# Kernel optimization log

Hardware: AMD Instinct MI355X
Metric: run time of the kernel (lower is better)

## Reference

```python
import jax, jax.numpy as jnp
import numpy as np
import math

N = 50000      # nodes
E = 800000     # edges
IN = 64        # in_channels
HID = 128      # hidden_channels
OUT = 64       # out_channels
RATIO = 0.8
K = int(math.ceil(RATIO * N))  # 40000 nodes kept after TopKPooling


def setup_inputs() -> dict:
    key = jax.random.key(0)
    ks = jax.random.split(key, 12)
    x = jax.random.normal(ks[0], (N, IN), jnp.float32)
    edge_index = jax.random.randint(ks[1], (2, E), 0, N, dtype=jnp.int32)
    batch = jnp.zeros((N,), jnp.int32)  # single graph

    def glorot(k, fi, fo):
        return jax.random.normal(k, (fi, fo), jnp.float32) * (1.0 / np.sqrt(fi))

    W1 = glorot(ks[2], IN, HID);  b1 = jnp.zeros((HID,), jnp.float32)
    pool_w = jax.random.normal(ks[3], (HID,), jnp.float32) * (1.0 / np.sqrt(HID))
    W2 = glorot(ks[4], HID, OUT); b2 = jnp.zeros((OUT,), jnp.float32)
    W3 = glorot(ks[5], OUT, HID); b3 = jnp.zeros((HID,), jnp.float32)
    W4 = glorot(ks[6], HID, IN);  b4 = jnp.zeros((IN,), jnp.float32)
    return dict(x=x, edge_index=edge_index, batch=batch,
                W1=W1, b1=b1, pool_w=pool_w, W2=W2, b2=b2,
                W3=W3, b3=b3, W4=W4, b4=b4)


def gcn_conv(x, src, dst, ew, W, b, n):
    """PyG GCNConv: D^{-1/2}(A+I)D^{-1/2} X W + b; ew is a 0/1 edge mask."""
    h = x @ W                                             # [n, d_out]
    deg = 1.0 + jax.ops.segment_sum(ew, dst, num_segments=n)  # self-loop adds 1
    dis = jax.lax.rsqrt(deg)
    norm = dis[src] * dis[dst] * ew                       # [E]
    agg = jax.ops.segment_sum(norm[:, None] * h[src], dst, num_segments=n)
    agg = agg + h * (dis * dis)[:, None]                  # self-loop: norm = 1/deg
    return agg + b


def reference(x, edge_index, batch, W1, b1, pool_w, W2, b2, W3, b3, W4, b4):
    src, dst = edge_index[0], edge_index[1]
    ew = jnp.ones((E,), x.dtype)

    # conv1 + relu
    h = jax.nn.relu(gcn_conv(x, src, dst, ew, W1, b1, N))

    # TopKPooling(ratio=0.8): score = tanh(x.w/||w||), keep top-K, scale x by score
    score = jnp.tanh(h @ pool_w / jnp.linalg.norm(pool_w))  # [N]
    vals, perm = jax.lax.top_k(score, K)
    hp = h[perm] * vals[:, None]                            # [K, HID]
    # remap edges to pooled node ids; drop edges touching removed nodes via mask
    new_idx = jnp.full((N,), -1, jnp.int32).at[perm].set(jnp.arange(K, dtype=jnp.int32))
    ns, nd = new_idx[src], new_idx[dst]
    valid = ((ns >= 0) & (nd >= 0)).astype(x.dtype)
    ns = jnp.maximum(ns, 0)
    nd = jnp.maximum(nd, 0)

    h2 = jax.nn.relu(gcn_conv(hp, ns, nd, valid, W2, b2, K))
    h3 = jax.nn.relu(gcn_conv(h2, ns, nd, valid, W3, b3, K))
    h4 = gcn_conv(h3, ns, nd, valid, W4, b4, K)             # [K, IN]

    # global_mean_pool over the (single) graph -> [1, IN]
    return jnp.mean(h4, axis=0, keepdims=True)
```

## Files before the change

kernel.cpp:

```cpp
#include <hip/hip_runtime.h>
#include <hip/hip_bf16.h>
#include <stdint.h>

#define N_NODES 50000
#define N_EDGES 800000
#define K_KEEP  40000
#define BKT     196
#define BCAP    6144

typedef unsigned long long u64;
typedef unsigned int u32;
typedef unsigned short u16;
typedef __hip_bfloat16 bf16;
typedef __hip_bfloat162 bf16x2;
typedef __attribute__((ext_vector_type(8))) short short8;
typedef __attribute__((ext_vector_type(8))) unsigned short ushort8;
typedef __attribute__((ext_vector_type(4))) float f32x4;

struct Ctl {
  u64 prefix;
  u32 kremain;
  u32 cnt;
  float inv_norm;
  u32 isfp32;
  u32 done;
  u32 pad;
  u32 gen;
  u32 done2;
  u32 hist[256];
};

__device__ __forceinline__ float bf2f(bf16 v) { return __bfloat162float(v); }
__device__ __forceinline__ float bfbits2f(unsigned short u) {
  return __uint_as_float(((u32)u) << 16);
}
__device__ __forceinline__ float loadF(const void* p, size_t i, bool f32) {
  return f32 ? ((const float*)p)[i] : bf2f(((const bf16*)p)[i]);
}
__device__ __forceinline__ short f2bf_bits(float f) {
  bf16 t = __float2bfloat16(f);
  return *(const short*)&t;
}

__device__ __forceinline__ void gather_row8_pre(const ushort8* __restrict__ H, int d, int lane,
                                                const int* __restrict__ rowstart,
                                                const int* __restrict__ len,
                                                const int* __restrict__ csr,
                                                float* acc)
{
  ushort8 v = H[(size_t)d * 8 + lane];
  #pragma unroll
  for (int c = 0; c < 8; ++c) acc[c] = bfbits2f(v[c]);
  int i = rowstart[d];
  int i1 = len ? (i + len[d]) : rowstart[d + 1];
  for (; i + 8 <= i1; i += 8) {
    int s0 = csr[i],     s1 = csr[i + 1], s2 = csr[i + 2], s3 = csr[i + 3];
    int s4 = csr[i + 4], s5 = csr[i + 5], s6 = csr[i + 6], s7 = csr[i + 7];
    ushort8 v0 = H[(size_t)s0 * 8 + lane];
    ushort8 v1 = H[(size_t)s1 * 8 + lane];
    ushort8 v2 = H[(size_t)s2 * 8 + lane];
    ushort8 v3 = H[(size_t)s3 * 8 + lane];
    ushort8 v4 = H[(size_t)s4 * 8 + lane];
    ushort8 v5 = H[(size_t)s5 * 8 + lane];
    ushort8 v6 = H[(size_t)s6 * 8 + lane];
    ushort8 v7 = H[(size_t)s7 * 8 + lane];
    #pragma unroll
    for (int c = 0; c < 8; ++c) {
      acc[c] += (bfbits2f(v0[c]) + bfbits2f(v1[c]))
              + (bfbits2f(v2[c]) + bfbits2f(v3[c]));
      acc[c] += (bfbits2f(v4[c]) + bfbits2f(v5[c]))
              + (bfbits2f(v6[c]) + bfbits2f(v7[c]));
    }
  }
  for (; i + 4 <= i1; i += 4) {
    int s0 = csr[i], s1 = csr[i + 1], s2 = csr[i + 2], s3 = csr[i + 3];
    ushort8 v0 = H[(size_t)s0 * 8 + lane];
    ushort8 v1 = H[(size_t)s1 * 8 + lane];
    ushort8 v2 = H[(size_t)s2 * 8 + lane];
    ushort8 v3 = H[(size_t)s3 * 8 + lane];
    #pragma unroll
    for (int c = 0; c < 8; ++c) {
      acc[c] += (bfbits2f(v0[c]) + bfbits2f(v1[c]))
              + (bfbits2f(v2[c]) + bfbits2f(v3[c]));
    }
  }
  for (; i < i1; ++i) {
    int s = csr[i];
    ushort8 vv = H[(size_t)s * 8 + lane];
    #pragma unroll
    for (int c = 0; c < 8; ++c) acc[c] += bfbits2f(vv[c]);
  }
}

__device__ __forceinline__ void gather_wave_partial(const ushort8* __restrict__ H, int d,
                                                    int slot, int unit,
                                                    const int* __restrict__ rowstart,
                                                    const int* __restrict__ len,
                                                    const int* __restrict__ csr,
                                                    float* acc,
                                                    float* __restrict__ cvec, float dd)
{
  #pragma unroll
  for (int c = 0; c < 8; ++c) acc[c] = 0.f;
  if (slot == 0) {
    ushort8 v = H[(size_t)d * 8 + unit];
    #pragma unroll
    for (int c = 0; c < 8; ++c) acc[c] = bfbits2f(v[c]);
  }
  int i0 = rowstart[d];
  int i1 = i0 + len[d];
  int i = i0 + slot;
  for (; i + 8 < i1; i += 16) {
    int sa = csr[i], sb = csr[i + 8];
    if (cvec && unit == 0) {
      atomicAdd(&cvec[sa], dd);
      atomicAdd(&cvec[sb], dd);
    }
    ushort8 va = H[(size_t)sa * 8 + unit];
    ushort8 vb = H[(size_t)sb * 8 + unit];
    #pragma unroll
    for (int c = 0; c < 8; ++c) acc[c] += bfbits2f(va[c]) + bfbits2f(vb[c]);
  }
  if (i < i1) {
    int s = csr[i];
    if (cvec && unit == 0) atomicAdd(&cvec[s], dd);
    ushort8 vv = H[(size_t)s * 8 + unit];
    #pragma unroll
    for (int c = 0; c < 8; ++c) acc[c] += bfbits2f(vv[c]);
  }
}


__global__ void init_kernel(const unsigned short* __restrict__ x16,
                            int* __restrict__ bucket_cur, int* __restrict__ detcnt,
                            Ctl* ctl, float* __restrict__ cvec) {
  __shared__ u32 dsh[256];
  int i = blockIdx.x * 256 + threadIdx.x;
  if (i < BKT) bucket_cur[i] = i * BCAP;
  if (i < K_KEEP) cvec[i] = 0.f;
  if (blockIdx.x == 0) {
    ctl->hist[threadIdx.x] = 0u;
    if (threadIdx.x == 0) {
      ctl->prefix = 0ull; ctl->kremain = K_KEEP; ctl->cnt = 0u;
      ctl->done = 0u; ctl->pad = 0u; ctl->gen = 0u; ctl->done2 = 0u;
    }
  }
  if (blockIdx.x < 64) {
    int base = blockIdx.x * 2048;
    u32 c = 0;
    for (int j = threadIdx.x; j < 2048; j += 256) {
      u32 h = x16[base + j];
      if ((h & 0x7F80u) == 0x7F80u) c++;
    }
    dsh[threadIdx.x] = c;
    __syncthreads();
    for (int s = 128; s > 0; s >>= 1) {
      if (threadIdx.x < s) dsh[threadIdx.x] += dsh[threadIdx.x + s];
      __syncthreads();
    }
    if (threadIdx.x == 0) detcnt[blockIdx.x] = (int)dsh[0];
  }
}


__global__ void bucket_scatter_kernel(const int* __restrict__ src, const int* __restrict__ dst,
                                      int* __restrict__ bucket_cur, u32* __restrict__ bucketbuf,
                                      const int* __restrict__ detcnt, const void* __restrict__ pw,
                                      Ctl* ctl)
{
  __shared__ u32 hist[BKT];
  __shared__ u32 base[BKT];
  __shared__ int f32sh;
  __shared__ float ns[128];
  const int tid = threadIdx.x;
  const int e0 = blockIdx.x * 2048;

  if (tid < 64) {
    int dc = detcnt[tid];
    for (int off = 32; off; off >>= 1) dc += __shfl_down(dc, off);
    if (tid == 0) f32sh = (dc >= 16) ? 1 : 0;
  }
  for (int t = tid; t < BKT; t += 256) hist[t] = 0;
  __syncthreads();
  const bool f32in = f32sh != 0;

  int dreg[8], sreg[8];
  const int eb = e0 + tid * 8;
  if (e0 + 2048 <= N_EDGES) {
    const int4* d4 = (const int4*)(dst + eb);
    const int4* s4 = (const int4*)(src + eb);
    int4 da = d4[0], db = d4[1];
    int4 sa = s4[0], sb = s4[1];
    dreg[0] = da.x; dreg[1] = da.y; dreg[2] = da.z; dreg[3] = da.w;
    dreg[4] = db.x; dreg[5] = db.y; dreg[6] = db.z; dreg[7] = db.w;
    sreg[0] = sa.x; sreg[1] = sa.y; sreg[2] = sa.z; sreg[3] = sa.w;
    sreg[4] = sb.x; sreg[5] = sb.y; sreg[6] = sb.z; sreg[7] = sb.w;
  } else {
    #pragma unroll
    for (int j = 0; j < 8; ++j) {
      int e = eb + j;
      if (e < N_EDGES) { dreg[j] = dst[e]; sreg[j] = src[e]; }
      else             { dreg[j] = -1;     sreg[j] = 0;      }
    }
  }
  #pragma unroll
  for (int j = 0; j < 8; ++j)
    if (dreg[j] >= 0) atomicAdd(&hist[dreg[j] >> 8], 1u);
  __syncthreads();
  for (int t = tid; t < BKT; t += 256) {
    u32 c = hist[t];
    base[t] = c ? (u32)atomicAdd(&bucket_cur[t], (int)c) : 0u;
    hist[t] = 0;
  }
  __syncthreads();
  #pragma unroll
  for (int j = 0; j < 8; ++j) {
    if (dreg[j] >= 0) {
      int d = dreg[j];
      int b = d >> 8;
      u32 pos = base[b] + atomicAdd(&hist[b], 1u);
      bucketbuf[pos] = ((u32)sreg[j] << 8) | (u32)(d & 255);
    }
  }
  if (blockIdx.x == 0) {
    if (tid < 128) { float v = loadF(pw, tid, f32in); ns[tid] = v * v; }
    __syncthreads();
    for (int s = 64; s > 0; s >>= 1) {
      if (tid < s) ns[tid] += ns[tid + s];
      __syncthreads();
    }
    if (tid == 0) {
      ctl->inv_norm = 1.0f / sqrtf(ns[0]);
      ctl->isfp32 = f32in ? 1u : 0u;
    }
  }
}


__global__ void csr_from_buckets_kernel(const u32* __restrict__ bucketbuf, const int* __restrict__ bucket_cur,
                                        int* __restrict__ rowstart, float* __restrict__ dis,
                                        int* __restrict__ csr,
                                        const void* __restrict__ x, ushort8* __restrict__ xbf,
                                        const Ctl* __restrict__ ctl)
{
  __shared__ u32 cnt[256];
  __shared__ u32 loc[256];
  __shared__ u32 cur[256];
  __shared__ float disS[256];
  const int b = blockIdx.x;
  const int tid = threadIdx.x;

  int v = (tid < BKT) ? (bucket_cur[tid] - tid * BCAP) : 0;
  loc[tid] = (u32)v;
  __syncthreads();
  for (int off = 1; off < 256; off <<= 1) {
    u32 t = (tid >= off) ? loc[tid - off] : 0;
    __syncthreads();
    loc[tid] += t;
    __syncthreads();
  }
  const int bc = bucket_cur[b] - b * BCAP;
  const int off0 = (int)loc[b] - bc;
  if (b == BKT - 1 && tid == 0) rowstart[N_NODES] = (int)loc[BKT - 1];
  __syncthreads();

  const u32* buf = bucketbuf + (size_t)b * BCAP;
  cnt[tid] = 0;
  __syncthreads();
  for (int i = tid; i < bc; i += 256) atomicAdd(&cnt[buf[i] & 255u], 1u);
  __syncthreads();
  u32 c = cnt[tid];
  loc[tid] = c;
  __syncthreads();
  for (int off = 1; off < 256; off <<= 1) {
    u32 t = (tid >= off) ? loc[tid - off] : 0;
    __syncthreads();
    loc[tid] += t;
    __syncthreads();
  }
  int node = b * 256 + tid;
  u32 excl = loc[tid] - c;
  float ddv = rsqrtf(1.0f + (float)c);
  disS[tid] = ddv;
  if (node < N_NODES) {
    rowstart[node] = off0 + (int)excl;
    dis[node] = ddv;
  }
  cur[tid] = off0 + excl;
  __syncthreads();
  for (int i = tid; i < bc; i += 256) {
    u32 p = buf[i];
    u32 pos = atomicAdd(&cur[p & 255u], 1u);
    csr[pos] = (int)(p >> 8);
  }
  {
    const bool f32in = ctl->isfp32 != 0;
    if (f32in) {
      const float* xf = (const float*)x;
      for (int u = tid; u < 2048; u += 256) {
        int r = u >> 3, lane = u & 7;
        int d = b * 256 + r;
        if (d < N_NODES) {
          float sc = disS[r];
          ushort8 o;
          #pragma unroll
          for (int c2 = 0; c2 < 8; ++c2)
            o[c2] = (u16)f2bf_bits(xf[(size_t)d * 64 + lane * 8 + c2] * sc);
          xbf[(size_t)d * 8 + lane] = o;
        }
      }
    } else {
      const ushort8* xi = (const ushort8*)x;
      for (int u = tid; u < 2048; u += 256) {
        int r = u >> 3, lane = u & 7;
        int d = b * 256 + r;
        if (d < N_NODES) {
          float sc = disS[r];
          ushort8 vv = xi[(size_t)d * 8 + lane];
          ushort8 o;
          #pragma unroll
          for (int c2 = 0; c2 < 8; ++c2)
            o[c2] = (u16)f2bf_bits(bfbits2f(vv[c2]) * sc);
          xbf[(size_t)d * 8 + lane] = o;
        }
      }
    }
  }
}


__global__ void gather_h2_kernel(const bf16* __restrict__ P, const int* __restrict__ rowstart,
                                 const int* __restrict__ len, const int* __restrict__ csr,
                                 const float* __restrict__ dis,
                                 const void* __restrict__ b, const Ctl* __restrict__ ctl,
                                 bf16* __restrict__ P2, float* __restrict__ cvec, int M)
{
  const bool f32 = ctl->isfp32 != 0;
  const int tid = threadIdx.x;
  const int d = blockIdx.x * 4 + (tid >> 6);
  const int lane = tid & 63;
  const int slot = lane >> 3, unit = lane & 7;
  const ushort8* H = (const ushort8*)P;
  const float dd = dis[d];
  float acc[8];
  gather_wave_partial(H, d, slot, unit, rowstart, len, csr, acc, cvec, dd);
  #pragma unroll
  for (int m = 8; m < 64; m <<= 1)
    #pragma unroll
    for (int c = 0; c < 8; ++c) acc[c] += __shfl_xor(acc[c], m);
  if (slot == 0) {
    ushort8 outv;
    #pragma unroll
    for (int c = 0; c < 8; ++c) {
      float h = acc[c] * dd + loadF(b, 8 * unit + c, f32);
      outv[c] = (u16)f2bf_bits(fmaxf(h, 0.f) * dd);
    }
    ((ushort8*)P2)[(size_t)d * 8 + unit] = outv;
  }
}


__global__ void gemm_in_kernel(const ushort8* __restrict__ xbf,
                               const int* __restrict__ rowstart, const int* __restrict__ csr,
                               const float* __restrict__ dis,
                               const void* __restrict__ W, const void* __restrict__ b,
                               const void* __restrict__ pw,
                               bf16* __restrict__ Y, const Ctl* __restrict__ ctl,
                               float* __restrict__ score, u64* __restrict__ keys)
{
  __shared__ short Xs[64 * 72];
  __shared__ short Wt[128 * 72];
  __shared__ float bs[128];
  __shared__ float ps[128];
  const bool f32 = ctl->isfp32 != 0;
  const int tid = threadIdx.x;
  const int row0 = blockIdx.x * 64;

  if (!f32) {
    const short8* W8 = (const short8*)W;
    for (int i = tid; i < 1024; i += 256) {
      int k = i >> 4, nb = i & 15;
      short8 v = W8[i];
      #pragma unroll
      for (int j = 0; j < 8; ++j) Wt[(nb * 8 + j) * 72 + k] = v[j];
    }
  } else {
    for (int i = tid; i < 64 * 128; i += 256) {
      int k = i >> 7, n = i & 127;
      Wt[n * 72 + k] = f2bf_bits(((const float*)W)[i]);
    }
  }
  for (int u = tid; u < 512; u += 256) {
    int r = u >> 3, lane = u & 7;
    int d = row0 + r;
    float acc[8];
    short8 outv;
    if (d < N_NODES) {
      gather_row8_pre(xbf, d, lane, rowstart, nullptr, csr, acc);
      float dd = dis[d];
      #pragma unroll
      for (int c = 0; c < 8; ++c) outv[c] = f2bf_bits(acc[c] * dd);
    } else {
      #pragma unroll
      for (int c = 0; c < 8; ++c) outv[c] = 0;
    }
    *(short8*)&Xs[r * 72 + lane * 8] = outv;
  }
  for (int i = tid; i < 128; i += 256) { bs[i] = loadF(b, i, f32); ps[i] = loadF(pw, i, f32); }
  __syncthreads();

  const int lane = tid & 63;
  const int w = tid >> 6;
  const int l16 = lane & 15;
  const int quad = lane >> 4;
  f32x4 acc[8];
  #pragma unroll
  for (int ct = 0; ct < 8; ++ct) acc[ct] = (f32x4){0.f, 0.f, 0.f, 0.f};
  const int arow = w * 16 + l16;
  #pragma unroll
  for (int kc = 0; kc < 2; ++kc) {
    short8 a = *(short8*)&Xs[arow * 72 + kc * 32 + quad * 8];
    #pragma unroll
    for (int ct = 0; ct < 8; ++ct) {
      short8 bb = *(short8*)&Wt[(ct * 16 + l16) * 72 + kc * 32 + quad * 8];
      acc[ct] = __builtin_amdgcn_mfma_f32_16x16x32_bf16(a, bb, acc[ct], 0, 0, 0);
    }
  }
  float inv_norm = ctl->inv_norm;
  #pragma unroll
  for (int r = 0; r < 4; ++r) {
    int gr = row0 + w * 16 + quad * 4 + r;
    float p = 0.f;
    #pragma unroll
    for (int ct = 0; ct < 8; ++ct) {
      int col = ct * 16 + l16;
      float h = acc[ct][r] + bs[col];
      if (gr < N_NODES) Y[(size_t)gr * 128 + col] = __float2bfloat16(h);
      p += fmaxf(h, 0.f) * ps[col];
    }
    p += __shfl_down(p, 8, 16);
    p += __shfl_down(p, 4, 16);
    p += __shfl_down(p, 2, 16);
    p += __shfl_down(p, 1, 16);
    if (l16 == 0 && gr < N_NODES) {
      float sc = tanhf(p * inv_norm);
      score[gr] = sc;
      u32 u = __float_as_uint(sc);
      u = (u & 0x80000000u) ? ~u : (u | 0x80000000u);
      keys[gr] = (((u64)u) << 16) | (u64)(0xFFFFu - (u32)gr);
    }
  }
}

__global__ void gemm_128_64_kernel(const bf16* __restrict__ X, const void* __restrict__ W,
                                   bf16* __restrict__ Y, const Ctl* __restrict__ ctl,
                                   int M, int relu_x,
                                   const int* __restrict__ kept, const float* __restrict__ score,
                                   const float* __restrict__ prescale)
{
  __shared__ short Xs[64 * 136];
  __shared__ short Wt[64 * 136];
  __shared__ int keptS[64];
  __shared__ float scS[64];
  const bool f32 = ctl->isfp32 != 0;
  const int tid = threadIdx.x;
  const int row0 = blockIdx.x * 64;

  if (kept) {
    for (int i = tid; i < 64; i += 256) {
      int o = kept[row0 + i];
      keptS[i] = o;
      scS[i] = score[o];
    }
  }
  __syncthreads();

  if (!f32) {
    const short8* W8 = (const short8*)W;
    for (int i = tid; i < 1024; i += 256) {
      int k = i >> 3, nb = i & 7;
      short8 v = W8[i];
      #pragma unroll
      for (int j = 0; j < 8; ++j) Wt[(nb * 8 + j) * 136 + k] = v[j];
    }
  } else {
    for (int i = tid; i < 128 * 64; i += 256) {
      int k = i >> 6, n = i & 63;
      Wt[n * 136 + k] = f2bf_bits(((const float*)W)[i]);
    }
  }
  const u32* X2 = (const u32*)X;
  for (int p = tid; p < 64 * 64; p += 256) {
    int r = p >> 6, kp = p & 63;
    int srow = kept ? keptS[r] : (row0 + r);
    u32 v = X2[(size_t)srow * 64 + kp];
    if (relu_x) {
      if (v & 0x8000u) v &= 0xFFFF0000u;
      if (v & 0x80000000u) v &= 0x0000FFFFu;
    }
    if (kept) {
      bf16x2 h = *(bf16x2*)&v;
      float s = scS[r];
      bf16x2 o;
      o.x = __float2bfloat16(fmaxf(bf2f(h.x), 0.f) * s);
      o.y = __float2bfloat16(fmaxf(bf2f(h.y), 0.f) * s);
      v = *(u32*)&o;
    }
    *(u32*)&Xs[r * 136 + 2 * kp] = v;
  }
  __syncthreads();

  const int lane = tid & 63;
  const int w = tid >> 6;
  const int l16 = lane & 15;
  const int quad = lane >> 4;
  f32x4 acc[4];
  #pragma unroll
  for (int ct = 0; ct < 4; ++ct) acc[ct] = (f32x4){0.f, 0.f, 0.f, 0.f};
  const int arow = w * 16 + l16;
  #pragma unroll
  for (int kc = 0; kc < 4; ++kc) {
    short8 a = *(short8*)&Xs[arow * 136 + kc * 32 + quad * 8];
    #pragma unroll
    for (int ct = 0; ct < 4; ++ct) {
      short8 bb = *(short8*)&Wt[(ct * 16 + l16) * 136 + kc * 32 + quad * 8];
      acc[ct] = __builtin_amdgcn_mfma_f32_16x16x32_bf16(a, bb, acc[ct], 0, 0, 0);
    }
  }
  #pragma unroll
  for (int ct = 0; ct < 4; ++ct)
    #pragma unroll
    for (int r = 0; r < 4; ++r) {
      int gr = row0 + w * 16 + quad * 4 + r;
      float val = acc[ct][r];
      if (prescale) val *= prescale[gr];
      Y[(size_t)gr * 64 + ct * 16 + l16] = __float2bfloat16(val);
    }
}

__global__ void gemm_64_128_kernel(const bf16* __restrict__ P2,
                                   const int* __restrict__ rowstart, const int* __restrict__ len,
                                   const int* __restrict__ csr, const float* __restrict__ dis,
                                   const void* __restrict__ W, const void* __restrict__ b,
                                   bf16* __restrict__ Y, const Ctl* __restrict__ ctl, int M)
{
  __shared__ short Xs[64 * 72];
  __shared__ short Wt[128 * 72];
  __shared__ float bs[128];
  const bool f32 = ctl->isfp32 != 0;
  const int tid = threadIdx.x;
  const int row0 = blockIdx.x * 64;

  if (!f32) {
    const short8* W8 = (const short8*)W;
    for (int i = tid; i < 1024; i += 256) {
      int k = i >> 4, nb = i & 15;
      short8 v = W8[i];
      #pragma unroll
      for (int j = 0; j < 8; ++j) Wt[(nb * 8 + j) * 72 + k] = v[j];
    }
  } else {
    for (int i = tid; i < 64 * 128; i += 256) {
      int k = i >> 7, n = i & 127;
      Wt[n * 72 + k] = f2bf_bits(((const float*)W)[i]);
    }
  }
  {
    const ushort8* H = (const ushort8*)P2;
    for (int u = tid; u < 512; u += 256) {
      int r = u >> 3, lane = u & 7;
      int d = row0 + r;
      float acc[8];
      gather_row8_pre(H, d, lane, rowstart, len, csr, acc);
      float dd = dis[d];
      short8 outv;
      #pragma unroll
      for (int c = 0; c < 8; ++c) outv[c] = f2bf_bits(acc[c] * dd);
      *(short8*)&Xs[r * 72 + lane * 8] = outv;
    }
  }
  for (int i = tid; i < 128; i += 256) bs[i] = loadF(b, i, f32);
  __syncthreads();

  const int lane = tid & 63;
  const int w = tid >> 6;
  const int l16 = lane & 15;
  const int quad = lane >> 4;
  f32x4 acc[8];
  #pragma unroll
  for (int ct = 0; ct < 8; ++ct) acc[ct] = (f32x4){0.f, 0.f, 0.f, 0.f};
  const int arow = w * 16 + l16;
  #pragma unroll
  for (int kc = 0; kc < 2; ++kc) {
    short8 a = *(short8*)&Xs[arow * 72 + kc * 32 + quad * 8];
    #pragma unroll
    for (int ct = 0; ct < 8; ++ct) {
      short8 bb = *(short8*)&Wt[(ct * 16 + l16) * 72 + kc * 32 + quad * 8];
      acc[ct] = __builtin_amdgcn_mfma_f32_16x16x32_bf16(a, bb, acc[ct], 0, 0, 0);
    }
  }
  #pragma unroll
  for (int ct = 0; ct < 8; ++ct)
    #pragma unroll
    for (int r = 0; r < 4; ++r) {
      int gr = row0 + w * 16 + quad * 4 + r;
      int col = ct * 16 + l16;
      Y[(size_t)gr * 128 + col] = __float2bfloat16(acc[ct][r] + bs[col]);
    }
}


__global__ void weighted_sum_kernel(const bf16* __restrict__ H3, const float* __restrict__ cvec,
                                    const float* __restrict__ dis,
                                    float* __restrict__ partial, int M, int nblk)
{
  __shared__ float cs[128];
  const int tid = threadIdx.x;
  if (tid < 128) cs[tid] = 0.f;
  __syncthreads();
  const int lane = tid & 15;
  const ushort8* H = (const ushort8*)H3;
  float acc[8];
  #pragma unroll
  for (int c = 0; c < 8; ++c) acc[c] = 0.f;
  for (int r = (blockIdx.x * 256 + tid) >> 4; r < M; r += nblk * 16) {
    float wgt = dis[r] * cvec[r];
    ushort8 v = H[(size_t)r * 16 + lane];
    #pragma unroll
    for (int c = 0; c < 8; ++c) acc[c] += wgt * fmaxf(bfbits2f(v[c]), 0.f);
  }
  #pragma unroll
  for (int c = 0; c < 8; ++c) atomicAdd(&cs[8 * lane + c], acc[c]);
  __syncthreads();
  if (tid < 128) partial[(size_t)tid * nblk + blockIdx.x] = cs[tid];
}

__global__ void final_out_kernel(const float* __restrict__ partial, const void* __restrict__ W4,
                                 const void* __restrict__ b4, const Ctl* __restrict__ ctl,
                                 void* __restrict__ out, int nblk)
{
  __shared__ float red[512];
  __shared__ float S[128];
  const int tid = threadIdx.x;
  {
    const int ch = tid >> 2, chunk = tid & 3;
    const int per = nblk / 4;
    float s = 0.f;
    const float* p = partial + (size_t)ch * nblk + chunk * per;
    for (int j = 0; j < per; j += 4)
      s += (p[j] + p[j + 1]) + (p[j + 2] + p[j + 3]);
    red[tid] = s;
  }
  __syncthreads();
  if (tid < 128) S[tid] = (red[4 * tid] + red[4 * tid + 1]) + (red[4 * tid + 2] + red[4 * tid + 3]);
  __syncthreads();
  {
    const bool f32 = ctl->isfp32 != 0;
    const int c = tid >> 3, chunk = tid & 7;
    float o = 0.f;
    #pragma unroll
    for (int j = 0; j < 16; ++j) {
      int k = chunk * 16 + j;
      o += S[k] * loadF(W4, (size_t)k * 64 + c, f32);
    }
    red[tid] = o;
    __syncthreads();
    if (tid < 64) {
      float acc = 0.f;
      #pragma unroll
      for (int j = 0; j < 8; ++j) acc += red[tid * 8 + j];
      float val = acc / (float)K_KEEP + loadF(b4, tid, f32);
      if (f32) ((float*)out)[tid] = val;
      else     ((bf16*)out)[tid] = __float2bfloat16(val);
    }
  }
}


__device__ __forceinline__ void mark_slice(const u64* __restrict__ keys, Ctl* ctl,
                                           int* __restrict__ new_idx, int* __restrict__ kept,
                                           int i)
{
  if (i >= N_NODES) return;
  if (keys[i] >= ctl->prefix) {
    int pos = (int)atomicAdd(&ctl->cnt, 1u);
    new_idx[i] = pos;
    kept[pos] = i;
  } else {
    new_idx[i] = -1;
  }
}

__global__ void histpick_kernel(const u64* __restrict__ keys, Ctl* ctl, int shift, int pass,
                                int nblocks, int* __restrict__ new_idx, int* __restrict__ kept) {
  __shared__ u32 lh[256];
  __shared__ u32 sfx[256];
  __shared__ int lastflag;
  __shared__ int selsh;
  const int tid = threadIdx.x;
  const u32 g = ctl->gen;
  if (g != 0u) {
    if ((u32)pass == g)
      mark_slice(keys, ctl, new_idx, kept, blockIdx.x * 256 + tid);
    return;
  }
  lh[tid] = 0;
  __syncthreads();
  u64 prefix = ctl->prefix;
  int i = blockIdx.x * 256 + tid;
  if (i < N_NODES) {
    u64 key = keys[i];
    if ((key >> (shift + 8)) == (prefix >> (shift + 8)))
      atomicAdd(&lh[(u32)((key >> shift) & 0xFF)], 1u);
  }
  __syncthreads();
  u32 c = lh[tid];
  if (c) atomicAdd(&ctl->hist[tid], c);
  __syncthreads();
  if (tid == 0) {
    __threadfence();
    u32 old = atomicAdd(&ctl->done, 1u);
    lastflag = (old == (u32)(nblocks - 1));
  }
  __syncthreads();
  if (!lastflag) return;
  u32 cc = atomicExch(&ctl->hist[tid], 0u);
  sfx[tid] = cc;
  __syncthreads();
  for (int off = 1; off < 256; off <<= 1) {
    u32 t = (tid + off < 256) ? sfx[tid + off] : 0u;
    __syncthreads();
    sfx[tid] += t;
    __syncthreads();
  }
  u32 kr = ctl->kremain;
  u32 above = (tid < 255) ? sfx[tid + 1] : 0u;
  if (sfx[tid] >= kr && above < kr) selsh = tid;
  __syncthreads();
  if (tid == 0) {
    int sel = selsh;
    u32 ab = (sel < 255) ? sfx[sel + 1] : 0u;
    u32 newkr = kr - ab;
    u32 bucketcnt = sfx[sel] - ab;
    ctl->kremain = newkr;
    ctl->prefix = prefix | (((u64)(u32)sel) << shift);
    if (newkr == bucketcnt) ctl->gen = (u32)(pass + 1);
    ctl->done = 0u;
  }
}

__global__ void mark_kernel(const u64* __restrict__ keys, Ctl* ctl,
                            int* __restrict__ new_idx, int* __restrict__ kept)
{
  u32 g = ctl->gen;
  if (g >= 1u && g <= 5u) return;
  mark_slice(keys, ctl, new_idx, kept, blockIdx.x * 256 + (int)threadIdx.x);
}


__global__ void csr2_build_kernel(const int* __restrict__ kept, const int* __restrict__ rowstart1,
                                  const int* __restrict__ csr1, const int* __restrict__ new_idx,
                                  Ctl* ctl, int* __restrict__ rowstart2, int* __restrict__ len2,
                                  float* __restrict__ dis2, int* __restrict__ csr2,
                                  float* __restrict__ cvec)
{
  int kp = blockIdx.x * 256 + threadIdx.x;
  int lane = threadIdx.x & 63;
  int c = 0;
  int i0 = 0, i1 = 0;
  if (kp < K_KEEP) {
    int o = kept[kp];
    i0 = rowstart1[o]; i1 = rowstart1[o + 1];
    int i = i0;
    for (; i + 8 <= i1; i += 8) {
      int s0 = csr1[i],     s1 = csr1[i + 1], s2 = csr1[i + 2], s3 = csr1[i + 3];
      int s4 = csr1[i + 4], s5 = csr1[i + 5], s6 = csr1[i + 6], s7 = csr1[i + 7];
      c += (new_idx[s0] >= 0) + (new_idx[s1] >= 0) + (new_idx[s2] >= 0) + (new_idx[s3] >= 0)
         + (new_idx[s4] >= 0) + (new_idx[s5] >= 0) + (new_idx[s6] >= 0) + (new_idx[s7] >= 0);
    }
    for (; i < i1; ++i) c += (new_idx[csr1[i]] >= 0);
  }
  int pre = c;
  #pragma unroll
  for (int off = 1; off < 64; off <<= 1) {
    int t = __shfl_up(pre, off);
    if (lane >= off) pre += t;
  }
  int wtot = __shfl(pre, 63);
  int wbase = 0;
  if (lane == 0) wbase = (int)atomicAdd(&ctl->pad, (u32)wtot);
  wbase = __shfl(wbase, 0);
  int base = wbase + pre - c;
  if (kp < K_KEEP) {
    rowstart2[kp] = base;
    len2[kp] = c;
    float ddv = rsqrtf(1.0f + (float)c);
    dis2[kp] = ddv;
    cvec[kp] = ddv;
    int w = base;
    int i = i0;
    for (; i + 4 <= i1; i += 4) {
      int n0 = new_idx[csr1[i]];
      int n1 = new_idx[csr1[i + 1]];
      int n2 = new_idx[csr1[i + 2]];
      int n3 = new_idx[csr1[i + 3]];
      if (n0 >= 0) csr2[w++] = n0;
      if (n1 >= 0) csr2[w++] = n1;
      if (n2 >= 0) csr2[w++] = n2;
      if (n3 >= 0) csr2[w++] = n3;
    }
    for (; i < i1; ++i) {
      int ns = new_idx[csr1[i]];
      if (ns >= 0) csr2[w++] = ns;
    }
  }
}


extern "C" void kernel_launch(void* const* d_in, const int* in_sizes, int n_in,
                              void* d_out, int out_size, void* d_ws, size_t ws_size,
                              hipStream_t stream)
{
  const void* x  = d_in[0];
  const int*  ei = (const int*)d_in[1];
  const void* W1 = d_in[3];
  const void* b1 = d_in[4];
  const void* pw = d_in[5];
  const void* W2 = d_in[6];
  const void* b2 = d_in[7];
  const void* W3 = d_in[8];
  const void* b3 = d_in[9];
  const void* W4 = d_in[10];
  const void* b4 = d_in[11];

  const int* src = ei;
  const int* dst = ei + N_EDGES;

  float* F = (float*)d_ws;
  bf16*  A16       = (bf16*)F;
  bf16*  B16       = (bf16*)(F + 3200000);
  bf16*  C16       = (bf16*)(F + 6400000);
  u32*   xbf       = (u32*)(F + 9000000);
  float* dis1      = F + 10600000;
  float* dis2      = F + 10650000;
  float* score     = F + 10690000;
  u64*   keys      = (u64*)(F + 10740000);
  int*   new_idx   = (int*)(F + 10840000);
  int*   kept      = (int*)(F + 10890000);
  int*   len2      = (int*)(F + 10930000);
  int*   rowstart1 = (int*)(F + 10970000);
  int*   rowstart2 = (int*)(F + 11020004);
  int*   csr1      = (int*)(F + 11060008);
  int*   csr2      = (int*)(F + 11860008);
  Ctl*   ctl       = (Ctl*)(F + 12660008);
  int*   detcnt    = (int*)(F + 12660856);
  int*   bucket_cur= (int*)(F + 12660920);
  float* cvec      = F + 12665216;
  u32*   bucketbuf = (u32*)(F + 12726908);
  float* partial   = F + 13931132;

  const int NB1 = (N_NODES + 255) / 256;
  const int EB2 = (N_EDGES + 2047) / 2048;
  const int GB1 = (N_NODES + 63) / 64;
  const int WBK = K_KEEP / 4;
  const int CB2 = (K_KEEP + 255) / 256;
  const int NWS = 128;

  init_kernel<<<NB1, 256, 0, stream>>>((const unsigned short*)x, bucket_cur, detcnt, ctl, cvec);

  bucket_scatter_kernel<<<EB2, 256, 0, stream>>>(src, dst, bucket_cur, bucketbuf,
                                                 detcnt, pw, ctl);
  csr_from_buckets_kernel<<<BKT, 256, 0, stream>>>(bucketbuf, bucket_cur, rowstart1, dis1, csr1,
                                                   x, (ushort8*)xbf, ctl);

  gemm_in_kernel<<<GB1, 256, 0, stream>>>((const ushort8*)xbf, rowstart1, csr1, dis1,
                                          W1, b1, pw, B16, ctl, score, keys);

  for (int p = 0; p < 6; ++p)
    histpick_kernel<<<NB1, 256, 0, stream>>>(keys, ctl, 40 - 8 * p, p, NB1, new_idx, kept);
  mark_kernel<<<NB1, 256, 0, stream>>>(keys, ctl, new_idx, kept);

  csr2_build_kernel<<<CB2, 256, 0, stream>>>(kept, rowstart1, csr1, new_idx, ctl,
                                             rowstart2, len2, dis2, csr2, cvec);

  gemm_128_64_kernel<<<K_KEEP / 64, 256, 0, stream>>>(B16, W2, A16, ctl, K_KEEP, 0, kept, score, dis2);
  gather_h2_kernel<<<WBK, 256, 0, stream>>>(A16, rowstart2, len2, csr2, dis2, b2, ctl, C16, cvec, K_KEEP);

  gemm_64_128_kernel<<<K_KEEP / 64, 256, 0, stream>>>(C16, rowstart2, len2, csr2, dis2,
                                                      W3, b3, B16, ctl, K_KEEP);

  weighted_sum_kernel<<<NWS, 256, 0, stream>>>(B16, cvec, dis2, partial, K_KEEP, NWS);
  final_out_kernel<<<1, 512, 0, stream>>>(partial, W4, b4, ctl, d_out, NWS);
}
```

Baseline: 285.8 us.

## Fuse weighted column sum into GEMM epilogue and parallelize CSR2 build per row

The 64x128 GEMM now reduces its output tile in its epilogue into per-block partial column sums, weighted by dis*cvec after bf16 rounding and ReLU, instead of writing H3 and running a separate weighted-sum kernel. This removes an intermediate write and read of a K x 128 bf16 array and one launch. The final reduction now handles a non-multiple-of-4 count of partials, 625 instead of 128. Separately, CSR2 construction uses 8 lanes per kept row, with shuffle reductions and ballot-based compaction, to spread the irregular edge loops over more threads.

```diff
diff --git a/kernel.cpp b/kernel.cpp
--- a/kernel.cpp
+++ b/kernel.cpp
@@ -542,15 +542,24 @@
                                    const int* __restrict__ rowstart, const int* __restrict__ len,
                                    const int* __restrict__ csr, const float* __restrict__ dis,
                                    const void* __restrict__ W, const void* __restrict__ b,
-                                   bf16* __restrict__ Y, const Ctl* __restrict__ ctl, int M)
+                                   const float* __restrict__ cvec,
+                                   float* __restrict__ partial,
+                                   const Ctl* __restrict__ ctl, int M, int nblk)
 {
   __shared__ short Xs[64 * 72];
   __shared__ short Wt[128 * 72];
   __shared__ float bs[128];
+  __shared__ float wgtS[64];
+  __shared__ float cs[128];
   const bool f32 = ctl->isfp32 != 0;
   const int tid = threadIdx.x;
   const int row0 = blockIdx.x * 64;
 
+  if (tid < 128) cs[tid] = 0.f;
+  if (tid < 64) {
+    int gr = row0 + tid;
+    wgtS[tid] = dis[gr] * cvec[gr];
+  }
   if (!f32) {
     const short8* W8 = (const short8*)W;
     for (int i = tid; i < 1024; i += 256) {
@@ -600,37 +609,18 @@
     }
   }
   #pragma unroll
-  for (int ct = 0; ct < 8; ++ct)
+  for (int ct = 0; ct < 8; ++ct) {
+    int col = ct * 16 + l16;
+    float s = 0.f;
     #pragma unroll
     for (int r = 0; r < 4; ++r) {
-      int gr = row0 + w * 16 + quad * 4 + r;
-      int col = ct * 16 + l16;
-      Y[(size_t)gr * 128 + col] = __float2bfloat16(acc[ct][r] + bs[col]);
-    }
-}
-
-
-__global__ void weighted_sum_kernel(const bf16* __restrict__ H3, const float* __restrict__ cvec,
-                                    const float* __restrict__ dis,
-                                    float* __restrict__ partial, int M, int nblk)
-{
-  __shared__ float cs[128];
-  const int tid = threadIdx.x;
-  if (tid < 128) cs[tid] = 0.f;
-  __syncthreads();
-  const int lane = tid & 15;
-  const ushort8* H = (const ushort8*)H3;
-  float acc[8];
-  #pragma unroll
-  for (int c = 0; c < 8; ++c) acc[c] = 0.f;
-  for (int r = (blockIdx.x * 256 + tid) >> 4; r < M; r += nblk * 16) {
-    float wgt = dis[r] * cvec[r];
-    ushort8 v = H[(size_t)r * 16 + lane];
-    #pragma unroll
-    for (int c = 0; c < 8; ++c) acc[c] += wgt * fmaxf(bfbits2f(v[c]), 0.f);
-  }
-  #pragma unroll
-  for (int c = 0; c < 8; ++c) atomicAdd(&cs[8 * lane + c], acc[c]);
+      int lr = w * 16 + quad * 4 + r;
+      float h = acc[ct][r] + bs[col];
+      float hb = bfbits2f((u16)f2bf_bits(h));
+      s += fmaxf(hb, 0.f) * wgtS[lr];
+    }
+    atomicAdd(&cs[col], s);
+  }
   __syncthreads();
   if (tid < 128) partial[(size_t)tid * nblk + blockIdx.x] = cs[tid];
 }
@@ -644,11 +634,10 @@
   const int tid = threadIdx.x;
   {
     const int ch = tid >> 2, chunk = tid & 3;
-    const int per = nblk / 4;
+    const int per = (nblk + 3) / 4;
     float s = 0.f;
-    const float* p = partial + (size_t)ch * nblk + chunk * per;
-    for (int j = 0; j < per; j += 4)
-      s += (p[j] + p[j + 1]) + (p[j + 2] + p[j + 3]);
+    const float* p = partial + (size_t)ch * nblk;
+    for (int j = chunk * per; j < (chunk + 1) * per && j < nblk; ++j) s += p[j];
     red[tid] = s;
   }
   __syncthreads();
@@ -764,54 +753,49 @@
                                   float* __restrict__ dis2, int* __restrict__ csr2,
                                   float* __restrict__ cvec)
 {
-  int kp = blockIdx.x * 256 + threadIdx.x;
-  int lane = threadIdx.x & 63;
+  const int gid = blockIdx.x * 256 + threadIdx.x;
+  const int kp = gid >> 3;
+  const int lane = threadIdx.x & 63;
+  const int grp = lane >> 3, l8 = lane & 7;
   int c = 0;
   int i0 = 0, i1 = 0;
   if (kp < K_KEEP) {
     int o = kept[kp];
     i0 = rowstart1[o]; i1 = rowstart1[o + 1];
-    int i = i0;
-    for (; i + 8 <= i1; i += 8) {
-      int s0 = csr1[i],     s1 = csr1[i + 1], s2 = csr1[i + 2], s3 = csr1[i + 3];
-      int s4 = csr1[i + 4], s5 = csr1[i + 5], s6 = csr1[i + 6], s7 = csr1[i + 7];
-      c += (new_idx[s0] >= 0) + (new_idx[s1] >= 0) + (new_idx[s2] >= 0) + (new_idx[s3] >= 0)
-         + (new_idx[s4] >= 0) + (new_idx[s5] >= 0) + (new_idx[s6] >= 0) + (new_idx[s7] >= 0);
-    }
-    for (; i < i1; ++i) c += (new_idx[csr1[i]] >= 0);
-  }
-  int pre = c;
-  #pragma unroll
-  for (int off = 1; off < 64; off <<= 1) {
-    int t = __shfl_up(pre, off);
-    if (lane >= off) pre += t;
-  }
-  int wtot = __shfl(pre, 63);
+    for (int i = i0 + l8; i < i1; i += 8) c += (new_idx[csr1[i]] >= 0);
+  }
+  c += __shfl_xor(c, 1);
+  c += __shfl_xor(c, 2);
+  c += __shfl_xor(c, 4);
+  int pre = 0, wtot = 0;
+  #pragma unroll
+  for (int g = 0; g < 8; ++g) {
+    int tg = __shfl(c, g * 8);
+    if (g < grp) pre += tg;
+    wtot += tg;
+  }
   int wbase = 0;
   if (lane == 0) wbase = (int)atomicAdd(&ctl->pad, (u32)wtot);
   wbase = __shfl(wbase, 0);
-  int base = wbase + pre - c;
+  int w = wbase + pre;
   if (kp < K_KEEP) {
-    rowstart2[kp] = base;
-    len2[kp] = c;
-    float ddv = rsqrtf(1.0f + (float)c);
-    dis2[kp] = ddv;
-    cvec[kp] = ddv;
-    int w = base;
-    int i = i0;
-    for (; i + 4 <= i1; i += 4) {
-      int n0 = new_idx[csr1[i]];
-      int n1 = new_idx[csr1[i + 1]];
-      int n2 = new_idx[csr1[i + 2]];
-      int n3 = new_idx[csr1[i + 3]];
-      if (n0 >= 0) csr2[w++] = n0;
-      if (n1 >= 0) csr2[w++] = n1;
-      if (n2 >= 0) csr2[w++] = n2;
-      if (n3 >= 0) csr2[w++] = n3;
-    }
-    for (; i < i1; ++i) {
-      int ns = new_idx[csr1[i]];
-      if (ns >= 0) csr2[w++] = ns;
+    if (l8 == 0) {
+      rowstart2[kp] = w;
+      len2[kp] = c;
+      float ddv = rsqrtf(1.0f + (float)c);
+      dis2[kp] = ddv;
+      cvec[kp] = ddv;
+    }
+    for (int ib = i0; ib < i1; ib += 8) {
+      int i = ib + l8;
+      int ns = (i < i1) ? new_idx[csr1[i]] : -1;
+      u64 bal = __ballot(ns >= 0);
+      u32 m8 = (u32)((bal >> (grp * 8)) & 0xFFull);
+      if (ns >= 0) {
+        int rank = __popc(m8 & ((1u << l8) - 1u));
+        csr2[w + rank] = ns;
+      }
+      w += __popc(m8);
     }
   }
 }
@@ -863,8 +847,8 @@
   const int EB2 = (N_EDGES + 2047) / 2048;
   const int GB1 = (N_NODES + 63) / 64;
   const int WBK = K_KEEP / 4;
-  const int CB2 = (K_KEEP + 255) / 256;
-  const int NWS = 128;
+  const int CB8 = K_KEEP * 8 / 256;
+  const int GB3 = K_KEEP / 64;
 
   init_kernel<<<NB1, 256, 0, stream>>>((const unsigned short*)x, bucket_cur, detcnt, ctl, cvec);
 
@@ -880,15 +864,14 @@
     histpick_kernel<<<NB1, 256, 0, stream>>>(keys, ctl, 40 - 8 * p, p, NB1, new_idx, kept);
   mark_kernel<<<NB1, 256, 0, stream>>>(keys, ctl, new_idx, kept);
 
-  csr2_build_kernel<<<CB2, 256, 0, stream>>>(kept, rowstart1, csr1, new_idx, ctl,
+  csr2_build_kernel<<<CB8, 256, 0, stream>>>(kept, rowstart1, csr1, new_idx, ctl,
                                              rowstart2, len2, dis2, csr2, cvec);
 
   gemm_128_64_kernel<<<K_KEEP / 64, 256, 0, stream>>>(B16, W2, A16, ctl, K_KEEP, 0, kept, score, dis2);
   gather_h2_kernel<<<WBK, 256, 0, stream>>>(A16, rowstart2, len2, csr2, dis2, b2, ctl, C16, cvec, K_KEEP);
 
-  gemm_64_128_kernel<<<K_KEEP / 64, 256, 0, stream>>>(C16, rowstart2, len2, csr2, dis2,
-                                                      W3, b3, B16, ctl, K_KEEP);
-
-  weighted_sum_kernel<<<NWS, 256, 0, stream>>>(B16, cvec, dis2, partial, K_KEEP, NWS);
-  final_out_kernel<<<1, 512, 0, stream>>>(partial, W4, b4, ctl, d_out, NWS);
-}
+  gemm_64_128_kernel<<<GB3, 256, 0, stream>>>(C16, rowstart2, len2, csr2, dis2,
+                                              W3, b3, cvec, partial, ctl, K_KEEP, GB3);
+
+  final_out_kernel<<<1, 512, 0, stream>>>(partial, W4, b4, ctl, d_out, GB3);
+}
```

Result: slower. 385.9 us (+35.0%).
